# Optimization experiments

Hardware: AMD Instinct MI355X
Metric: run time of the kernel (lower is better)

The kernel has to match this reference:

```python
import jax, jax.numpy as jnp
import numpy as np

GAMMA = 1.0        # soft-min temperature for differentiable DTW
BIG = 1e9          # value for cells outside the Sakoe-Chiba band
DTW_BW = 0.2       # band width as fraction of normalized path deviation
AVG_T_LEN = True   # divide discrepancy by input sequence length


def _softmin3(a, b, c):
    # differentiable min over the three DP predecessors
    z = jnp.stack([a, b, c], axis=0)
    return -GAMMA * jax.nn.logsumexp(-z / GAMMA, axis=0)


def _dtw(C, mask):
    """Band-limited soft-DTW DP. C: [T,K] pairwise costs, mask: [T,K] bool band.
    Returns scalar D[T-1,K-1]. Row scan over T; inner scan over K carries the
    left neighbor (recurrence D[i,j] = C[i,j] + softmin(D[i-1,j], D[i,j-1], D[i-1,j-1]))."""
    T, K = C.shape

    def row_step(carry, inp):
        prev_row, diag0 = carry            # prev_row: D[i-1,:]; diag0: virtual D[i-1,-1]
        c_row, m_row = inp
        diag = jnp.concatenate([diag0[None], prev_row[:-1]])  # D[i-1,j-1]

        def col_step(left, xs):
            c, up, dg, m = xs
            d = c + _softmin3(up, left, dg)
            d = jnp.where(m, d, BIG)       # kill cells outside the band
            return d, d

        _, row = jax.lax.scan(col_step, jnp.float32(BIG), (c_row, prev_row, diag, m_row))
        return (row, jnp.float32(BIG)), None

    # virtual border: D[-1,-1] = 0, all other border cells = BIG
    init = (jnp.full((K,), BIG, dtype=jnp.float32), jnp.float32(0.0))
    (last_row, _), _ = jax.lax.scan(row_step, init, (C, mask))
    return last_row[-1]


def setup_inputs() -> dict:
    key = jax.random.key(0)
    kx, kp = jax.random.split(key)
    B, T = 64, 512
    F, K = 32, 64
    x = jax.random.normal(kx, (B, T), dtype=jnp.float32)
    protos = jax.random.normal(kp, (F, K), dtype=jnp.float32)  # learnable DTW kernels
    return {"x": x, "protos": protos}


def reference(x, protos):
    B, T = x.shape
    F, K = protos.shape
    # pairwise squared costs: [B, F, T, K]
    C = (x[:, None, :, None] - protos[None, :, None, :]) ** 2
    # Sakoe-Chiba band on normalized coordinates
    ii = jnp.arange(T, dtype=jnp.float32) / (T - 1)
    jj = jnp.arange(K, dtype=jnp.float32) / (K - 1)
    mask = jnp.abs(ii[:, None] - jj[None, :]) <= DTW_BW  # [T, K]
    d = jax.vmap(jax.vmap(lambda c: _dtw(c, mask)))(C)    # [B, F]
    if AVG_T_LEN:
        d = d / jnp.float32(T)
    return d[:, :, None]  # [B, num_filter, out_len=1]
```

## Files before the change

### kernel.cpp

```cpp
#include <hip/hip_runtime.h>

#define T_LEN  512
#define K_LEN  64
#define NFILT  32
#define NBATCH 64
#define XOFS   64
#define XS_SZ  640
#define CHUNK  32
#define SQRT_LOG2E 1.2011224087864498f
#define LN2        0.6931471805599453f

typedef __attribute__((ext_vector_type(2))) float f32x2;

static __device__ __forceinline__ float wave_shr1(float x) {
    int r = __builtin_amdgcn_update_dpp(0, __builtin_bit_cast(int, x),
                                        0x138, 0xF, 0xF, true);
    return __builtin_bit_cast(float, r);
}

static __device__ __forceinline__ f32x2 wave_shr1_x2(f32x2 v) {
    f32x2 r;
    r.x = wave_shr1(v.x);
    r.y = wave_shr1(v.y);
    return r;
}

template <int N>
static __device__ __forceinline__ float row_ror(float x) {
    int r = __builtin_amdgcn_update_dpp(0, __builtin_bit_cast(int, x),
                                        0x120 + N, 0xF, 0xF, true);
    return __builtin_bit_cast(float, r);
}

static __device__ __forceinline__ float exp2_fast(float x) {
#if __has_builtin(__builtin_amdgcn_exp2f)
    return __builtin_amdgcn_exp2f(x);
#else
    return exp2f(x);
#endif
}

__global__ __launch_bounds__(256) void dtw_kernel(const float* __restrict__ x,
                                                  const float* __restrict__ protos,
                                                  float* __restrict__ out) {
    __shared__ float xs[XS_SZ];
    const int tid  = threadIdx.x;
    const int lane = tid & 63;
    const int wid  = tid >> 6;
    const int b    = blockIdx.x >> 2;
    const int fA   = ((blockIdx.x & 3) << 2) | wid;
    const int fB   = fA + 16;

    for (int t0 = tid; t0 < XS_SZ; t0 += 256) {
        int i = t0 - XOFS;
        xs[t0] = (i >= 0 && i < T_LEN) ? x[b * T_LEN + i] * SQRT_LOG2E : 0.0f;
    }
    __syncthreads();

    const float pAn = -protos[fA * K_LEN + lane] * SQRT_LOG2E;
    const float pBn = -protos[fB * K_LEN + lane] * SQRT_LOG2E;
    const float jj  = (float)lane / 63.0f;

    int a0 = 0, b0 = T_LEN - 1;
    while (a0 < b0) { int m = (a0 + b0) >> 1;
        if ((float)m / 511.0f - jj >= -0.2f) b0 = m; else a0 = m + 1; }
    const int ilo = a0;
    a0 = 0; b0 = T_LEN - 1;
    while (a0 < b0) { int m = (a0 + b0 + 1) >> 1;
        if ((float)m / 511.0f - jj <= 0.2f) a0 = m; else b0 = m - 1; }
    const int ihi = a0;

    const unsigned range = (unsigned)(ihi - ilo);
    unsigned t = (unsigned)(-(lane + ilo));
    f32x2 prev2 = {0.0f, 0.0f};
    const float d0 = (lane == 0) ? 1.0f : 0.0f;
    f32x2 dgp2 = {d0, d0};
    int   S2A = 0, S2B = 0;
    int   base = XOFS - lane;

    float A[CHUNK], Bv[CHUNK];
#pragma unroll
    for (int k = 0; k < CHUNK; ++k) A[k] = xs[base + k];
    __builtin_amdgcn_sched_barrier(0);

#define STEP(XV) do {                                         \
        float xv_  = (XV);                                    \
        float sel_ = (t <= range) ? 0.0f : -3.0e38f;          \
        ++t;                                                  \
        float dA_ = xv_ + pAn;    \
        float dB_ = xv_ + pBn;                                \
        f32x2 w2_;                                            \
        w2_.x = exp2_fast(__builtin_fmaf(dA_, -dA_, sel_));   \
        w2_.y = exp2_fast(__builtin_fmaf(dB_, -dB_, sel_));   \
        f32x2 l2_ = wave_shr1_x2(prev2);                      \
        f32x2 a2_ = prev2 + dgp2;           \
        f32x2 s2_ = a2_ + l2_;              \
        dgp2  = l2_;                                          \
        prev2 = s2_ * w2_;                  \
    } while (0)

#define RENORM() do {                                                        \
        float MA_, MB_;                                                      \
        {                                                                    \
            float m_ = prev2.x;                                              \
            m_ = fmaxf(m_, row_ror<8>(m_));                                  \
            m_ = fmaxf(m_, row_ror<4>(m_));                                  \
            m_ = fmaxf(m_, row_ror<2>(m_));                                  \
            m_ = fmaxf(m_, row_ror<1>(m_));                                  \
            int mi_ = __builtin_bit_cast(int, m_);                           \
            unsigned r0_ = (unsigned)__builtin_amdgcn_readlane(mi_, 0);      \
            unsigned r1_ = (unsigned)__builtin_amdgcn_readlane(mi_, 16);     \
            unsigned r2_ = (unsigned)__builtin_amdgcn_readlane(mi_, 32);     \
            unsigned r3_ = (unsigned)__builtin_amdgcn_readlane(mi_, 48);     \
            unsigned ra_ = r0_ > r1_ ? r0_ : r1_;                            \
            unsigned rb_ = r2_ > r3_ ? r2_ : r3_;                            \
            unsigned mx_ = ra_ > rb_ ? ra_ : rb_;                            \
            int e_  = (int)((mx_ >> 23) & 0xFF);                             \
            int Me_ = 284 - e_;                                              \
            Me_ = Me_ < 1 ? 1 : (Me_ > 254 ? 254 : Me_);                     \
            MA_ = __builtin_bit_cast(float, Me_ << 23);                      \
            S2A += Me_ - 127;                                                \
        }                                                                    \
        {                                                                    \
            float m_ = prev2.y;                                              \
            m_ = fmaxf(m_, row_ror<8>(m_));                                  \
            m_ = fmaxf(m_, row_ror<4>(m_));                                  \
            m_ = fmaxf(m_, row_ror<2>(m_));                                  \
            m_ = fmaxf(m_, row_ror<1>(m_));                                  \
            int mi_ = __builtin_bit_cast(int, m_);                           \
            unsigned r0_ = (unsigned)__builtin_amdgcn_readlane(mi_, 0);      \
            unsigned r1_ = (unsigned)__builtin_amdgcn_readlane(mi_, 16);     \
            unsigned r2_ = (unsigned)__builtin_amdgcn_readlane(mi_, 32);     \
            unsigned r3_ = (unsigned)__builtin_amdgcn_readlane(mi_, 48);     \
            unsigned ra_ = r0_ > r1_ ? r0_ : r1_;                            \
            unsigned rb_ = r2_ > r3_ ? r2_ : r3_;                            \
            unsigned mx_ = ra_ > rb_ ? ra_ : rb_;                            \
            int e_  = (int)((mx_ >> 23) & 0xFF);                             \
            int Me_ = 284 - e_;                                              \
            Me_ = Me_ < 1 ? 1 : (Me_ > 254 ? 254 : Me_);                     \
            MB_ = __builtin_bit_cast(float, Me_ << 23);                      \
            S2B += Me_ - 127;                                                \
        }                                                                    \
        f32x2 M2_ = {MA_, MB_};                                              \
        prev2 = prev2 * M2_;                               \
        dgp2  = dgp2  * M2_;                               \
    } while (0)

#pragma unroll 1
    for (int cc = 0; cc < 8; ++cc) {
#pragma unroll
        for (int k = 0; k < CHUNK; ++k) Bv[k] = xs[base + CHUNK + k];
        __builtin_amdgcn_sched_barrier(0);
#pragma unroll
        for (int k = 0; k < CHUNK; ++k) STEP(A[k]);
        RENORM();
        __builtin_amdgcn_sched_barrier(0);
        base += CHUNK;
#pragma unroll
        for (int k = 0; k < CHUNK; ++k) A[k] = xs[base + CHUNK + k];
        __builtin_amdgcn_sched_barrier(0);
#pragma unroll
        for (int k = 0; k < CHUNK; ++k) STEP(Bv[k]);
        RENORM();
        __builtin_amdgcn_sched_barrier(0);
        base += CHUNK;
    }
#pragma unroll
    for (int k = 0; k < CHUNK; ++k) Bv[k] = xs[base + CHUNK + k];
    __builtin_amdgcn_sched_barrier(0);
#pragma unroll
    for (int k = 0; k < CHUNK; ++k) STEP(A[k]);
    RENORM();
#pragma unroll
    for (int k = 0; k < 31; ++k) STEP(Bv[k]);

    if (lane == 63) {
        float DA = ((float)S2A - log2f(prev2.x)) * LN2;
        float DB = ((float)S2B - log2f(prev2.y)) * LN2;
        out[b * NFILT + fA] = DA * (1.0f / (float)T_LEN);
        out[b * NFILT + fB] = DB * (1.0f / (float)T_LEN);
    }
#undef STEP
#undef RENORM
}

extern "C" void kernel_launch(void* const* d_in, const int* in_sizes, int n_in,
                              void* d_out, int out_size, void* d_ws, size_t ws_size,
                              hipStream_t stream) {
    const float* x      = (const float*)d_in[0];
    const float* protos = (const float*)d_in[1];
    float* out          = (float*)d_out;

    dim3 grid(NBATCH * 4);
    dim3 block(256);
    hipLaunchKernelGGL(dtw_kernel, grid, block, 0, stream, x, protos, out);
}
```

Baseline: 27.54 us.

## Split soft-DTW into forward and backward half-sweeps meeting at middle

```diff
diff --git a/kernel.cpp b/kernel.cpp
--- a/kernel.cpp
+++ b/kernel.cpp
@@ -4,9 +4,8 @@
 #define K_LEN  64
 #define NFILT  32
 #define NBATCH 64
-#define XOFS   64
-#define XS_SZ  640
-#define CHUNK  32
+#define XOFS2  64
+#define XS2_SZ 384
 #define SQRT_LOG2E 1.2011224087864498f
 #define LN2        0.6931471805599453f
 
@@ -40,63 +39,91 @@
 #endif
 }
 
+static __device__ __forceinline__ void band_iv(float jj, int& lo, int& hi) {
+    int a0 = 0, b0 = T_LEN - 1;
+    while (a0 < b0) { int m = (a0 + b0) >> 1;
+        if ((float)m / 511.0f - jj >= -0.2f) b0 = m; else a0 = m + 1; }
+    lo = a0;
+    a0 = 0; b0 = T_LEN - 1;
+    while (a0 < b0) { int m = (a0 + b0 + 1) >> 1;
+        if ((float)m / 511.0f - jj <= 0.2f) a0 = m; else b0 = m - 1; }
+    hi = a0;
+}
+
 __global__ __launch_bounds__(256) void dtw_kernel(const float* __restrict__ x,
                                                   const float* __restrict__ protos,
                                                   float* __restrict__ out) {
-    __shared__ float xs[XS_SZ];
+    __shared__ f32x2 xs2[XS2_SZ];
     const int tid  = threadIdx.x;
     const int lane = tid & 63;
     const int wid  = tid >> 6;
-    const int b    = blockIdx.x >> 2;
-    const int fA   = ((blockIdx.x & 3) << 2) | wid;
-    const int fB   = fA + 16;
-
-    for (int t0 = tid; t0 < XS_SZ; t0 += 256) {
-        int i = t0 - XOFS;
-        xs[t0] = (i >= 0 && i < T_LEN) ? x[b * T_LEN + i] * SQRT_LOG2E : 0.0f;
+    const int idx  = (blockIdx.x << 2) | wid;
+    const int b    = idx >> 5;
+    const int f    = idx & 31;
+
+    for (int t0 = tid; t0 < XS2_SZ; t0 += 256) {
+        int i = t0 - XOFS2;
+        f32x2 v;
+        bool ok = (i >= 0 && i < T_LEN);
+        v.x = ok ? x[b * T_LEN + i] * SQRT_LOG2E : 0.0f;
+        v.y = ok ? x[b * T_LEN + (T_LEN - 1) - i] * SQRT_LOG2E : 0.0f;
+        xs2[t0] = v;
     }
     __syncthreads();
 
-    const float pAn = -protos[fA * K_LEN + lane] * SQRT_LOG2E;
-    const float pBn = -protos[fB * K_LEN + lane] * SQRT_LOG2E;
-    const float jj  = (float)lane / 63.0f;
-
-    int a0 = 0, b0 = T_LEN - 1;
-    while (a0 < b0) { int m = (a0 + b0) >> 1;
-        if ((float)m / 511.0f - jj >= -0.2f) b0 = m; else a0 = m + 1; }
-    const int ilo = a0;
-    a0 = 0; b0 = T_LEN - 1;
-    while (a0 < b0) { int m = (a0 + b0 + 1) >> 1;
-        if ((float)m / 511.0f - jj <= 0.2f) a0 = m; else b0 = m - 1; }
-    const int ihi = a0;
-
-    const unsigned range = (unsigned)(ihi - ilo);
-    unsigned t = (unsigned)(-(lane + ilo));
-    f32x2 prev2 = {0.0f, 0.0f};
+    const int jF = lane, jB = 63 - lane;
+    f32x2 pn2;
+    pn2.x = -protos[f * K_LEN + jF] * SQRT_LOG2E;
+    pn2.y = -protos[f * K_LEN + jB] * SQRT_LOG2E;
+
+    int iloF, ihiF, iloB, ihiB;
+    band_iv((float)jF / 63.0f, iloF, ihiF);
+    band_iv((float)jB / 63.0f, iloB, ihiB);
+
+    const int loF = iloF, hiF = (ihiF < 255) ? ihiF : 255;
+    const int loBo = (iloB > 256) ? iloB : 256;
+    const int loB  = (T_LEN - 1) - ihiB;
+    const int hiB  = (T_LEN - 1) - loBo;
+
+    unsigned tF, rangeF, tB, rangeB;
+    if (loF > hiF) { tF = 0x80000000u; rangeF = 0u; }
+    else { tF = (unsigned)(-(lane + loF)); rangeF = (unsigned)(hiF - loF); }
+    if (loB > hiB) { tB = 0x80000000u; rangeB = 0u; }
+    else { tB = (unsigned)(-(lane + loB)); rangeB = (unsigned)(hiB - loB); }
+
+    f32x2 prev2; prev2.x = 0.0f; prev2.y = 0.0f;
+    f32x2 cap2;  cap2.x  = 0.0f; cap2.y  = 0.0f;
     const float d0 = (lane == 0) ? 1.0f : 0.0f;
-    f32x2 dgp2 = {d0, d0};
-    int   S2A = 0, S2B = 0;
-    int   base = XOFS - lane;
-
-    float A[CHUNK], Bv[CHUNK];
+    f32x2 dgp2; dgp2.x = d0; dgp2.y = d0;
+    int S2x = 0, S2y = 0;
+    const int dcap = 255 + lane;
+
+    const f32x2* __restrict__ xp = &xs2[XOFS2 - lane];
+
+    f32x2 A[32], Bv[32];
 #pragma unroll
-    for (int k = 0; k < CHUNK; ++k) A[k] = xs[base + k];
+    for (int k = 0; k < 32; ++k) A[k] = xp[k];
     __builtin_amdgcn_sched_barrier(0);
 
-#define STEP(XV) do {                                         \
-        float xv_  = (XV);                                    \
-        float sel_ = (t <= range) ? 0.0f : -3.0e38f;          \
-        ++t;                                                  \
-        float dA_ = xv_ + pAn;    \
-        float dB_ = xv_ + pBn;                                \
+#define STEP(XV, DCONST, CAPF) do {                           \
+        f32x2 xv2_ = (XV);                                    \
+        float selF_ = (tF <= rangeF) ? 0.0f : -3.0e38f; ++tF; \
+        float selB_ = (tB <= rangeB) ? 0.0f : -3.0e38f; ++tB; \
+        float dF_ = xv2_.x + pn2.x;                           \
+        float dB_ = xv2_.y + pn2.y;                           \
         f32x2 w2_;                                            \
-        w2_.x = exp2_fast(__builtin_fmaf(dA_, -dA_, sel_));   \
-        w2_.y = exp2_fast(__builtin_fmaf(dB_, -dB_, sel_));   \
+        w2_.x = exp2_fast(__builtin_fmaf(dF_, -dF_, selF_));  \
+        w2_.y = exp2_fast(__builtin_fmaf(dB_, -dB_, selB_));  \
         f32x2 l2_ = wave_shr1_x2(prev2);                      \
-        f32x2 a2_ = prev2 + dgp2;           \
-        f32x2 s2_ = a2_ + l2_;              \
+        f32x2 a2_ = prev2 + dgp2;                             \
+        f32x2 s2_ = a2_ + l2_;                                \
         dgp2  = l2_;                                          \
-        prev2 = s2_ * w2_;                  \
+        prev2 = s2_ * w2_;                                    \
+        if (CAPF) {                                           \
+            bool c_ = (dcap == (DCONST));                     \
+            cap2.x = c_ ? prev2.x : cap2.x;                   \
+            cap2.y = c_ ? prev2.y : cap2.y;                   \
+        }                                                     \
     } while (0)
 
 #define RENORM() do {                                                        \
@@ -119,7 +146,7 @@
             int Me_ = 284 - e_;                                              \
             Me_ = Me_ < 1 ? 1 : (Me_ > 254 ? 254 : Me_);                     \
             MA_ = __builtin_bit_cast(float, Me_ << 23);                      \
-            S2A += Me_ - 127;                                                \
+            S2x += Me_ - 127;                                                \
         }                                                                    \
         {                                                                    \
             float m_ = prev2.y;                                              \
@@ -139,49 +166,102 @@
             int Me_ = 284 - e_;                                              \
             Me_ = Me_ < 1 ? 1 : (Me_ > 254 ? 254 : Me_);                     \
             MB_ = __builtin_bit_cast(float, Me_ << 23);                      \
-            S2B += Me_ - 127;                                                \
+            S2y += Me_ - 127;                                                \
         }                                                                    \
-        f32x2 M2_ = {MA_, MB_};                                              \
-        prev2 = prev2 * M2_;                               \
-        dgp2  = dgp2  * M2_;                               \
+        f32x2 M2_; M2_.x = MA_; M2_.y = MB_;                                 \
+        prev2 = prev2 * M2_;                                                 \
+        dgp2  = dgp2  * M2_;                                                 \
+        cap2  = cap2  * M2_;                                                 \
     } while (0)
 
-#pragma unroll 1
-    for (int cc = 0; cc < 8; ++cc) {
+#define CHUNKRUN(CBASE, CUR, NXT, CAPF) do {                                 \
+        _Pragma("unroll")                                                    \
+        for (int k = 0; k < 32; ++k) NXT[k] = xp[(CBASE) + 32 + k];          \
+        __builtin_amdgcn_sched_barrier(0);                                   \
+        _Pragma("unroll")                                                    \
+        for (int k = 0; k < 32; ++k) STEP(CUR[k], (CBASE) + k, CAPF);        \
+        RENORM();                                                            \
+        __builtin_amdgcn_sched_barrier(0);                                   \
+    } while (0)
+
+    CHUNKRUN(  0, A,  Bv, 0);
+    CHUNKRUN( 32, Bv, A,  0);
+    CHUNKRUN( 64, A,  Bv, 0);
+    CHUNKRUN( 96, Bv, A,  0);
+    CHUNKRUN(128, A,  Bv, 0);
+    CHUNKRUN(160, Bv, A,  0);
+    CHUNKRUN(192, A,  Bv, 0);
+    CHUNKRUN(224, Bv, A,  1);
+    CHUNKRUN(256, A,  Bv, 1);
 #pragma unroll
-        for (int k = 0; k < CHUNK; ++k) Bv[k] = xs[base + CHUNK + k];
-        __builtin_amdgcn_sched_barrier(0);
-#pragma unroll
-        for (int k = 0; k < CHUNK; ++k) STEP(A[k]);
-        RENORM();
-        __builtin_amdgcn_sched_barrier(0);
-        base += CHUNK;
-#pragma unroll
-        for (int k = 0; k < CHUNK; ++k) A[k] = xs[base + CHUNK + k];
-        __builtin_amdgcn_sched_barrier(0);
-#pragma unroll
-        for (int k = 0; k < CHUNK; ++k) STEP(Bv[k]);
-        RENORM();
-        __builtin_amdgcn_sched_barrier(0);
-        base += CHUNK;
+    for (int k = 0; k < 31; ++k) STEP(Bv[k], 288 + k, 1);
+
+    {
+        float MA_, MB_;
+        {
+            float m_ = cap2.x;
+            m_ = fmaxf(m_, row_ror<8>(m_));
+            m_ = fmaxf(m_, row_ror<4>(m_));
+            m_ = fmaxf(m_, row_ror<2>(m_));
+            m_ = fmaxf(m_, row_ror<1>(m_));
+            int mi_ = __builtin_bit_cast(int, m_);
+            unsigned r0_ = (unsigned)__builtin_amdgcn_readlane(mi_, 0);
+            unsigned r1_ = (unsigned)__builtin_amdgcn_readlane(mi_, 16);
+            unsigned r2_ = (unsigned)__builtin_amdgcn_readlane(mi_, 32);
+            unsigned r3_ = (unsigned)__builtin_amdgcn_readlane(mi_, 48);
+            unsigned ra_ = r0_ > r1_ ? r0_ : r1_;
+            unsigned rb_ = r2_ > r3_ ? r2_ : r3_;
+            unsigned mx_ = ra_ > rb_ ? ra_ : rb_;
+            int e_  = (int)((mx_ >> 23) & 0xFF);
+            int Me_ = 254 - e_;
+            Me_ = Me_ < 1 ? 1 : (Me_ > 254 ? 254 : Me_);
+            MA_ = __builtin_bit_cast(float, Me_ << 23);
+            S2x += Me_ - 127;
+        }
+        {
+            float m_ = cap2.y;
+            m_ = fmaxf(m_, row_ror<8>(m_));
+            m_ = fmaxf(m_, row_ror<4>(m_));
+            m_ = fmaxf(m_, row_ror<2>(m_));
+            m_ = fmaxf(m_, row_ror<1>(m_));
+            int mi_ = __builtin_bit_cast(int, m_);
+            unsigned r0_ = (unsigned)__builtin_amdgcn_readlane(mi_, 0);
+            unsigned r1_ = (unsigned)__builtin_amdgcn_readlane(mi_, 16);
+            unsigned r2_ = (unsigned)__builtin_amdgcn_readlane(mi_, 32);
+            unsigned r3_ = (unsigned)__builtin_amdgcn_readlane(mi_, 48);
+            unsigned ra_ = r0_ > r1_ ? r0_ : r1_;
+            unsigned rb_ = r2_ > r3_ ? r2_ : r3_;
+            unsigned mx_ = ra_ > rb_ ? ra_ : rb_;
+            int e_  = (int)((mx_ >> 23) & 0xFF);
+            int Me_ = 254 - e_;
+            Me_ = Me_ < 1 ? 1 : (Me_ > 254 ? 254 : Me_);
+            MB_ = __builtin_bit_cast(float, Me_ << 23);
+            S2y += Me_ - 127;
+        }
+        f32x2 M2_; M2_.x = MA_; M2_.y = MB_;
+        cap2 = cap2 * M2_;
     }
-#pragma unroll
-    for (int k = 0; k < CHUNK; ++k) Bv[k] = xs[base + CHUNK + k];
-    __builtin_amdgcn_sched_barrier(0);
-#pragma unroll
-    for (int k = 0; k < CHUNK; ++k) STEP(A[k]);
-    RENORM();
-#pragma unroll
-    for (int k = 0; k < 31; ++k) STEP(Bv[k]);
+    float cbj  = __shfl(cap2.y, 63 - lane);
+    float cbj1 = __shfl(cap2.y, 62 - lane);
+    float s = cap2.x * (cbj + cbj1);
+    float m = s;
+    m += row_ror<8>(m);
+    m += row_ror<4>(m);
+    m += row_ror<2>(m);
+    m += row_ror<1>(m);
+    int mi = __builtin_bit_cast(int, m);
+    float tot = m;
+    tot += __builtin_bit_cast(float, __builtin_amdgcn_readlane(mi, 0));
+    tot += __builtin_bit_cast(float, __builtin_amdgcn_readlane(mi, 16));
+    tot += __builtin_bit_cast(float, __builtin_amdgcn_readlane(mi, 32));
 
     if (lane == 63) {
-        float DA = ((float)S2A - log2f(prev2.x)) * LN2;
-        float DB = ((float)S2B - log2f(prev2.y)) * LN2;
-        out[b * NFILT + fA] = DA * (1.0f / (float)T_LEN);
-        out[b * NFILT + fB] = DB * (1.0f / (float)T_LEN);
+        float D = ((float)(S2x + S2y) - log2f(tot)) * LN2;
+        out[b * NFILT + f] = D * (1.0f / (float)T_LEN);
     }
 #undef STEP
 #undef RENORM
+#undef CHUNKRUN
 }
 
 extern "C" void kernel_launch(void* const* d_in, const int* in_sizes, int n_in,
@@ -191,7 +271,7 @@
     const float* protos = (const float*)d_in[1];
     float* out          = (float*)d_out;
 
-    dim3 grid(NBATCH * 4);
+    dim3 grid(512);
     dim3 block(256);
     hipLaunchKernelGGL(dtw_kernel, grid, block, 0, stream, x, protos, out);
 }
```

Result: slower. 34.05 us (+23.6%).
